# Kernel optimization log

Measured on AMD Instinct MI355X. Metric: run time of the kernel, lower is better.

## Reference

```python
import jax, jax.numpy as jnp
import numpy as np

D_MODEL = 1024
NUM_HEADS = 16
D_K = D_MODEL // NUM_HEADS


def setup_inputs() -> dict:
    key = jax.random.key(0)
    ks = jax.random.split(key, 11)
    B, S, D = 4, 2048, D_MODEL
    scale = 1.0 / np.sqrt(D)
    return {
        "Q": jax.random.normal(ks[0], (B, S, D), jnp.float32),
        "K": jax.random.normal(ks[1], (B, S, D), jnp.float32),
        "V": jax.random.normal(ks[2], (B, S, D), jnp.float32),
        "Wq": jax.random.normal(ks[3], (D, D), jnp.float32) * scale,
        "bq": jnp.zeros((D,), jnp.float32),
        "Wk": jax.random.normal(ks[4], (D, D), jnp.float32) * scale,
        "bk": jnp.zeros((D,), jnp.float32),
        "Wv": jax.random.normal(ks[5], (D, D), jnp.float32) * scale,
        "bv": jnp.zeros((D,), jnp.float32),
        "Wo": jax.random.normal(ks[6], (D, D), jnp.float32) * scale,
        "bo": jnp.zeros((D,), jnp.float32),
    }


def reference(Q, K, V, Wq, bq, Wk, bk, Wv, bv, Wo, bo):
    B, S, D = Q.shape
    H, Dk = NUM_HEADS, D_K
    # projections: [B,S,D] -> [B,H,S,Dk]
    def proj(x, W, b):
        y = jnp.einsum('bsd,de->bse', x, W.T) + b  # torch Linear: x @ W.T + b
        return y.reshape(B, -1, H, Dk).transpose(0, 2, 1, 3)
    q = proj(Q, Wq, bq)
    k = proj(K, Wk, bk)
    v = proj(V, Wv, bv)
    scores = jnp.einsum('bhqd,bhkd->bhqk', q, k) / np.sqrt(Dk)  # [B,H,S,S]
    attn = jax.nn.softmax(scores, axis=-1)
    out = jnp.einsum('bhqk,bhkd->bhqd', attn, v)  # [B,H,S,Dk]
    out = out.transpose(0, 2, 1, 3).reshape(B, -1, D)
    return jnp.einsum('bsd,de->bse', out, Wo.T) + bo
```

## Files before the change

kernel.cpp:

```cpp
#include <hip/hip_runtime.h>


typedef __bf16 bhalf_t;
typedef __attribute__((ext_vector_type(8)))  __bf16 bf16x8;
typedef __attribute__((ext_vector_type(4)))  __bf16 bf16x4;
typedef __attribute__((ext_vector_type(4)))  float  f32x4;
typedef __attribute__((ext_vector_type(16))) float  f32x16;

typedef __attribute__((address_space(1))) void gvoid_t;
typedef __attribute__((address_space(3))) void lvoid_t;
#define GLD16(g, l) __builtin_amdgcn_global_load_lds((const gvoid_t*)(g), (lvoid_t*)(l), 16, 0, 0)

__global__ __launch_bounds__(256) void cvt_all(
    const float* __restrict__ Q, const float* __restrict__ Kin, const float* __restrict__ V,
    const float* __restrict__ Wq, const float* __restrict__ Wk, const float* __restrict__ Wv,
    const float* __restrict__ Wo,
    bhalf_t* __restrict__ Qb, bhalf_t* __restrict__ Kb, bhalf_t* __restrict__ Vb,
    bhalf_t* __restrict__ Wqb, bhalf_t* __restrict__ Wkb, bhalf_t* __restrict__ Wvb,
    bhalf_t* __restrict__ Wob)
{
  size_t t = (size_t)blockIdx.x * 256 + threadIdx.x;
  const float* src; bhalf_t* dst;
  if (t < 2097152)      { src = Q;   dst = Qb; }
  else if (t < 4194304) { src = Kin; dst = Kb; t -= 2097152; }
  else if (t < 6291456) { src = V;   dst = Vb; t -= 4194304; }
  else {
    t -= 6291456;
    int w = (int)(t >> 18); t &= 262143;
    src = (w == 0) ? Wq  : (w == 1) ? Wk  : (w == 2) ? Wv  : Wo;
    dst = (w == 0) ? Wqb : (w == 1) ? Wkb : (w == 2) ? Wvb : Wob;
  }
  float4 f = ((const float4*)src)[t];
  bf16x4 o;
  o.x = (bhalf_t)f.x; o.y = (bhalf_t)f.y; o.z = (bhalf_t)f.z; o.w = (bhalf_t)f.w;
  ((bf16x4*)dst)[t] = o;
}

__device__ __forceinline__ void gemm_core_128(
    const bhalf_t* __restrict__ A, const bhalf_t* __restrict__ B,
    int bm, int bn, bhalf_t* As, bhalf_t* Bs, f32x4 acc[4][4])
{
  const int tid = threadIdx.x, lane = tid & 63, wave = tid >> 6;
  const int wm = wave >> 1, wn = wave & 1;
  const int quad = lane >> 4, tn = lane & 15;
  const int srow = lane >> 2, scol = (lane & 3) * 8;

  const bhalf_t* Ab0 = A + (size_t)(bm * 128 + wave * 16 + srow) * 1024 + scol;
  const bhalf_t* Ab1 = Ab0 + (size_t)64 * 1024;
  const bhalf_t* Bb0 = B + (size_t)(bn * 128 + wave * 16 + srow) * 1024 + scol;
  const bhalf_t* Bb1 = Bb0 + (size_t)64 * 1024;
  bhalf_t* Asw0 = As + wave * 512;  bhalf_t* Asw1 = As + (wave + 4) * 512;
  bhalf_t* Bsw0 = Bs + wave * 512;  bhalf_t* Bsw1 = Bs + (wave + 4) * 512;

  for (int k0 = 0; k0 < 1024; k0 += 32) {
    GLD16(Ab0 + k0, Asw0);
    GLD16(Ab1 + k0, Asw1);
    GLD16(Bb0 + k0, Bsw0);
    GLD16(Bb1 + k0, Bsw1);
    __syncthreads();
    bf16x8 af[4], bfr[4];
#pragma unroll
    for (int i = 0; i < 4; ++i)
      af[i] = *(const bf16x8*)(As + (wm * 64 + i * 16 + tn) * 32 + quad * 8);
#pragma unroll
    for (int j = 0; j < 4; ++j)
      bfr[j] = *(const bf16x8*)(Bs + (wn * 64 + j * 16 + tn) * 32 + quad * 8);
#pragma unroll
    for (int i = 0; i < 4; ++i)
#pragma unroll
      for (int j = 0; j < 4; ++j)
        acc[i][j] = __builtin_amdgcn_mfma_f32_16x16x32_bf16(af[i], bfr[j], acc[i][j], 0, 0, 0);
    __syncthreads();
  }
}

__global__ __launch_bounds__(256) void proj_gemm(
    const bhalf_t* __restrict__ Qb, const bhalf_t* __restrict__ Kb, const bhalf_t* __restrict__ Vb,
    const bhalf_t* __restrict__ Wqb, const bhalf_t* __restrict__ Wkb, const bhalf_t* __restrict__ Wvb,
    const float* __restrict__ bq, const float* __restrict__ bk, const float* __restrict__ bv,
    bhalf_t* __restrict__ qo, bhalf_t* __restrict__ ko, bhalf_t* __restrict__ vto)
{
  __shared__ bhalf_t As[4096];
  __shared__ bhalf_t Bs[4096];
  const int seg = blockIdx.x >> 9;
  const int idx = blockIdx.x & 511;
  const int bm = idx & 63, bn = idx >> 6;

  const bhalf_t *A, *Bw; const float* bias; bhalf_t* out; float scale; int mode;
  if (seg == 0)      { A = Qb; Bw = Wqb; bias = bq; out = qo;  scale = 0.18033688f; mode = 0; }
  else if (seg == 1) { A = Kb; Bw = Wkb; bias = bk; out = ko;  scale = 1.0f;        mode = 0; }
  else               { A = Vb; Bw = Wvb; bias = bv; out = vto; scale = 1.0f;        mode = 1; }

  f32x4 acc[4][4];
#pragma unroll
  for (int i = 0; i < 4; ++i)
#pragma unroll
    for (int j = 0; j < 4; ++j)
      acc[i][j] = (f32x4){0.f, 0.f, 0.f, 0.f};

  gemm_core_128(A, Bw, bm, bn, As, Bs, acc);

  const int lane = threadIdx.x & 63, wave = threadIdx.x >> 6;
  const int wm = wave >> 1, wn = wave & 1, quad = lane >> 4, tn = lane & 15;
#pragma unroll
  for (int i = 0; i < 4; ++i)
#pragma unroll
    for (int j = 0; j < 4; ++j) {
      const int n = bn * 128 + wn * 64 + j * 16 + tn;
      const float bsv = bias[n];
      const int h = n >> 6, dk = n & 63;
#pragma unroll
      for (int r = 0; r < 4; ++r) {
        const int m = bm * 128 + wm * 64 + i * 16 + quad * 4 + r;
        const int b = m >> 11, s = m & 2047;
        const float v = (acc[i][j][r] + bsv) * scale;
        size_t addr;
        if (mode == 0) addr = (((size_t)(b * 16 + h)) * 2048 + s) * 64 + dk;
        else {
          const int s2 = (s & ~12) | ((s & 4) << 1) | ((s & 8) >> 1);
          addr = (((size_t)(b * 16 + h)) * 64 + dk) * 2048 + s2;
        }
        out[addr] = (bhalf_t)v;
      }
    }
}

__global__ __launch_bounds__(256) void out_gemm(
    const bhalf_t* __restrict__ A, const bhalf_t* __restrict__ Bw,
    const float* __restrict__ bias, float* __restrict__ Cout)
{
  __shared__ bhalf_t As[4096];
  __shared__ bhalf_t Bs[4096];
  const int bm = blockIdx.x & 63, bn = blockIdx.x >> 6;

  f32x4 acc[4][4];
#pragma unroll
  for (int i = 0; i < 4; ++i)
#pragma unroll
    for (int j = 0; j < 4; ++j)
      acc[i][j] = (f32x4){0.f, 0.f, 0.f, 0.f};

  gemm_core_128(A, Bw, bm, bn, As, Bs, acc);

  const int lane = threadIdx.x & 63, wave = threadIdx.x >> 6;
  const int wm = wave >> 1, wn = wave & 1, quad = lane >> 4, tn = lane & 15;
#pragma unroll
  for (int i = 0; i < 4; ++i)
#pragma unroll
    for (int j = 0; j < 4; ++j) {
      const int n = bn * 128 + wn * 64 + j * 16 + tn;
      const float bsv = bias[n];
#pragma unroll
      for (int r = 0; r < 4; ++r) {
        const int m = bm * 128 + wm * 64 + i * 16 + quad * 4 + r;
        Cout[(size_t)m * 1024 + n] = acc[i][j][r] + bsv;
      }
    }
}

__global__ __launch_bounds__(256, 2) void attn_kernel(
    const bhalf_t* __restrict__ qp, const bhalf_t* __restrict__ kp,
    const bhalf_t* __restrict__ vtp, bhalf_t* __restrict__ outp)
{
  __shared__ bhalf_t Klds[4096];
  __shared__ bhalf_t Vtlds[4096];

  const int tid = threadIdx.x, lane = tid & 63, wave = tid >> 6;
  const int q31 = lane & 31, h = lane >> 5;
  const int bh = blockIdx.y, qt = blockIdx.x;

  const bhalf_t* qbase = qp + (((size_t)bh * 2048) + qt * 256 + wave * 64 + q31) * 64;
  bf16x8 qf[2][4];
#pragma unroll
  for (int qs = 0; qs < 2; ++qs)
#pragma unroll
    for (int ks = 0; ks < 4; ++ks)
      qf[qs][ks] = *(const bf16x8*)(qbase + qs * 32 * 64 + ks * 16 + h * 8);

  f32x16 Ot[2][2];
#pragma unroll
  for (int qs = 0; qs < 2; ++qs)
#pragma unroll
    for (int dd = 0; dd < 2; ++dd)
#pragma unroll
      for (int i = 0; i < 16; ++i) Ot[qs][dd][i] = 0.f;
  float Lp[2] = {0.f, 0.f};

  const bhalf_t* kbase  = kp  + (size_t)bh * 2048 * 64;
  const bhalf_t* vtbase = vtp + (size_t)bh * 64 * 2048;

  const int rloc = lane >> 3;
  const int cg8  = ((lane & 7) ^ rloc) * 8;
  const int q7 = q31 & 7;

  for (int kv0 = 0; kv0 < 2048; kv0 += 64) {
#pragma unroll
    for (int i = 0; i < 2; ++i) {
      const int r0 = (wave * 2 + i) * 8;
      GLD16(kbase + (size_t)(kv0 + r0 + rloc) * 64 + cg8, Klds + r0 * 64);
      GLD16(vtbase + (size_t)(r0 + rloc) * 2048 + kv0 + cg8, Vtlds + r0 * 64);
    }
    __syncthreads();

    bf16x8 pb[2][4];
#pragma unroll
    for (int mb = 0; mb < 2; ++mb) {
      bf16x8 ka[4];
#pragma unroll
      for (int ks = 0; ks < 4; ++ks)
        ka[ks] = *(const bf16x8*)(Klds + (mb * 32 + q31) * 64 + ((2 * ks + h) ^ q7) * 8);
#pragma unroll
      for (int qs = 0; qs < 2; ++qs) {
        f32x16 S;
#pragma unroll
        for (int i = 0; i < 16; ++i) S[i] = 0.f;
#pragma unroll
        for (int ks = 0; ks < 4; ++ks)
          S = __builtin_amdgcn_mfma_f32_32x32x16_bf16(ka[ks], qf[qs][ks], S, 0, 0, 0);
        float ls = 0.f;
#pragma unroll
        for (int half = 0; half < 2; ++half) {
          bf16x8 pk;
#pragma unroll
          for (int j = 0; j < 8; ++j) {
            const float e = __builtin_amdgcn_exp2f(S[half * 8 + j]);
            ls += e;
            pk[j] = (bhalf_t)e;
          }
          pb[qs][mb * 2 + half] = pk;
        }
        Lp[qs] += ls;
      }
    }

#pragma unroll
    for (int dd = 0; dd < 2; ++dd)
#pragma unroll
      for (int kb = 0; kb < 4; ++kb) {
        const bf16x8 va = *(const bf16x8*)(Vtlds + (dd * 32 + q31) * 64 + ((2 * kb + h) ^ q7) * 8);
#pragma unroll
        for (int qs = 0; qs < 2; ++qs)
          Ot[qs][dd] = __builtin_amdgcn_mfma_f32_32x32x16_bf16(va, pb[qs][kb], Ot[qs][dd], 0, 0, 0);
      }
    __syncthreads();
  }

  const int b = bh >> 4, hh = bh & 15;
#pragma unroll
  for (int qs = 0; qs < 2; ++qs) {
    const float Lt = Lp[qs] + __shfl_xor(Lp[qs], 32, 64);
    const float linv = 1.0f / Lt;
    const int s = qt * 256 + wave * 64 + qs * 32 + q31;
    bhalf_t* ob = outp + ((size_t)(b * 2048 + s)) * 1024 + hh * 64;
#pragma unroll
    for (int dd = 0; dd < 2; ++dd)
#pragma unroll
      for (int g = 0; g < 4; ++g) {
        bf16x4 o;
        o.x = (bhalf_t)(Ot[qs][dd][4 * g + 0] * linv);
        o.y = (bhalf_t)(Ot[qs][dd][4 * g + 1] * linv);
        o.z = (bhalf_t)(Ot[qs][dd][4 * g + 2] * linv);
        o.w = (bhalf_t)(Ot[qs][dd][4 * g + 3] * linv);
        *(bf16x4*)(ob + dd * 32 + g * 8 + h * 4) = o;
      }
  }
}

extern "C" void kernel_launch(void* const* d_in, const int* in_sizes, int n_in,
                              void* d_out, int out_size, void* d_ws, size_t ws_size,
                              hipStream_t stream)
{
  const float* Q  = (const float*)d_in[0];
  const float* K  = (const float*)d_in[1];
  const float* V  = (const float*)d_in[2];
  const float* Wq = (const float*)d_in[3];
  const float* bq = (const float*)d_in[4];
  const float* Wk = (const float*)d_in[5];
  const float* bk = (const float*)d_in[6];
  const float* Wv = (const float*)d_in[7];
  const float* bv = (const float*)d_in[8];
  const float* Wo = (const float*)d_in[9];
  const float* bo = (const float*)d_in[10];

  char* ws = (char*)d_ws;
  const size_t SZ = 8192ull * 1024 * 2;
  const size_t WZ = 1024ull * 1024 * 2;
  bhalf_t* Qb   = (bhalf_t*)(ws);
  bhalf_t* Kb   = (bhalf_t*)(ws + SZ);
  bhalf_t* Vb   = (bhalf_t*)(ws + 2 * SZ);
  bhalf_t* Wqb  = (bhalf_t*)(ws + 3 * SZ);
  bhalf_t* Wkb  = (bhalf_t*)(ws + 3 * SZ + WZ);
  bhalf_t* Wvb  = (bhalf_t*)(ws + 3 * SZ + 2 * WZ);
  bhalf_t* Wob  = (bhalf_t*)(ws + 3 * SZ + 3 * WZ);
  bhalf_t* q_p  = (bhalf_t*)(ws + 3 * SZ + 4 * WZ);
  bhalf_t* k_p  = (bhalf_t*)(ws + 4 * SZ + 4 * WZ);
  bhalf_t* vt_p = (bhalf_t*)(ws + 5 * SZ + 4 * WZ);
  bhalf_t* attn_o = Qb;

  cvt_all<<<28672, 256, 0, stream>>>(Q, K, V, Wq, Wk, Wv, Wo,
                                     Qb, Kb, Vb, Wqb, Wkb, Wvb, Wob);
  proj_gemm<<<1536, 256, 0, stream>>>(Qb, Kb, Vb, Wqb, Wkb, Wvb,
                                      bq, bk, bv, q_p, k_p, vt_p);
  attn_kernel<<<dim3(8, 64), 256, 0, stream>>>(q_p, k_p, vt_p, attn_o);
  out_gemm<<<512, 256, 0, stream>>>(attn_o, Wob, bo, (float*)d_out);
}
```

Before: 334.7 us.

## Fuse activation fp32->bf16 conversion into projection GEMM and double-buffer LDS

```diff
diff --git a/kernel.cpp b/kernel.cpp
--- a/kernel.cpp
+++ b/kernel.cpp
@@ -11,97 +11,102 @@
 typedef __attribute__((address_space(3))) void lvoid_t;
 #define GLD16(g, l) __builtin_amdgcn_global_load_lds((const gvoid_t*)(g), (lvoid_t*)(l), 16, 0, 0)
 
-__global__ __launch_bounds__(256) void cvt_all(
-    const float* __restrict__ Q, const float* __restrict__ Kin, const float* __restrict__ V,
-    const float* __restrict__ Wq, const float* __restrict__ Wk, const float* __restrict__ Wv,
-    const float* __restrict__ Wo,
-    bhalf_t* __restrict__ Qb, bhalf_t* __restrict__ Kb, bhalf_t* __restrict__ Vb,
-    bhalf_t* __restrict__ Wqb, bhalf_t* __restrict__ Wkb, bhalf_t* __restrict__ Wvb,
-    bhalf_t* __restrict__ Wob)
+__global__ __launch_bounds__(256) void cvt_w(
+    const float* __restrict__ Wq, const float* __restrict__ Wk,
+    const float* __restrict__ Wv, const float* __restrict__ Wo,
+    bhalf_t* __restrict__ Wqb, bhalf_t* __restrict__ Wkb,
+    bhalf_t* __restrict__ Wvb, bhalf_t* __restrict__ Wob)
 {
   size_t t = (size_t)blockIdx.x * 256 + threadIdx.x;
-  const float* src; bhalf_t* dst;
-  if (t < 2097152)      { src = Q;   dst = Qb; }
-  else if (t < 4194304) { src = Kin; dst = Kb; t -= 2097152; }
-  else if (t < 6291456) { src = V;   dst = Vb; t -= 4194304; }
-  else {
-    t -= 6291456;
-    int w = (int)(t >> 18); t &= 262143;
-    src = (w == 0) ? Wq  : (w == 1) ? Wk  : (w == 2) ? Wv  : Wo;
-    dst = (w == 0) ? Wqb : (w == 1) ? Wkb : (w == 2) ? Wvb : Wob;
-  }
+  int w = (int)(t >> 18); t &= 262143;
+  const float* src = (w == 0) ? Wq  : (w == 1) ? Wk  : (w == 2) ? Wv  : Wo;
+  bhalf_t*     dst = (w == 0) ? Wqb : (w == 1) ? Wkb : (w == 2) ? Wvb : Wob;
   float4 f = ((const float4*)src)[t];
   bf16x4 o;
   o.x = (bhalf_t)f.x; o.y = (bhalf_t)f.y; o.z = (bhalf_t)f.z; o.w = (bhalf_t)f.w;
   ((bf16x4*)dst)[t] = o;
 }
 
-__device__ __forceinline__ void gemm_core_128(
-    const bhalf_t* __restrict__ A, const bhalf_t* __restrict__ B,
-    int bm, int bn, bhalf_t* As, bhalf_t* Bs, f32x4 acc[4][4])
-{
+__global__ __launch_bounds__(256) void proj_gemm(
+    const float* __restrict__ Qf, const float* __restrict__ Kf, const float* __restrict__ Vf,
+    const bhalf_t* __restrict__ Wqb, const bhalf_t* __restrict__ Wkb, const bhalf_t* __restrict__ Wvb,
+    const float* __restrict__ bq, const float* __restrict__ bk, const float* __restrict__ bv,
+    bhalf_t* __restrict__ qo, bhalf_t* __restrict__ ko, bhalf_t* __restrict__ vto)
+{
+  __shared__ float   AsF[2][4096];
+  __shared__ bhalf_t Bs [2][4096];
+
+  const int seg = blockIdx.x >> 9;
+  const int idx = blockIdx.x & 511;
+  const int bm = idx & 63, bn = idx >> 6;
+
+  const float *A; const bhalf_t *Bw; const float* bias; bhalf_t* out; float scale; int mode;
+  if (seg == 0)      { A = Qf; Bw = Wqb; bias = bq; out = qo;  scale = 0.18033688f; mode = 0; }
+  else if (seg == 1) { A = Kf; Bw = Wkb; bias = bk; out = ko;  scale = 1.0f;        mode = 0; }
+  else               { A = Vf; Bw = Wvb; bias = bv; out = vto; scale = 1.0f;        mode = 1; }
+
   const int tid = threadIdx.x, lane = tid & 63, wave = tid >> 6;
   const int wm = wave >> 1, wn = wave & 1;
   const int quad = lane >> 4, tn = lane & 15;
-  const int srow = lane >> 2, scol = (lane & 3) * 8;
-
-  const bhalf_t* Ab0 = A + (size_t)(bm * 128 + wave * 16 + srow) * 1024 + scol;
-  const bhalf_t* Ab1 = Ab0 + (size_t)64 * 1024;
-  const bhalf_t* Bb0 = B + (size_t)(bn * 128 + wave * 16 + srow) * 1024 + scol;
-  const bhalf_t* Bb1 = Bb0 + (size_t)64 * 1024;
-  bhalf_t* Asw0 = As + wave * 512;  bhalf_t* Asw1 = As + (wave + 4) * 512;
-  bhalf_t* Bsw0 = Bs + wave * 512;  bhalf_t* Bsw1 = Bs + (wave + 4) * 512;
-
+
+  const int ar = lane >> 3;
+  const int ac = ((lane & 7) ^ ar) * 4;
+  const int br = lane >> 2;
+  const int bc = ((lane & 3) ^ (br & 3)) * 8;
+
+  const float*   Ag = A  + (size_t)(bm * 128 + ar) * 1024 + ac;
+  const bhalf_t* Bg = Bw + (size_t)(bn * 128 + br) * 1024 + bc;
+
+  auto stage = [&](int k0, int buf) {
+#pragma unroll
+    for (int i = 0; i < 4; ++i)
+      GLD16(Ag + (size_t)(wave * 32 + i * 8) * 1024 + k0, &AsF[buf][(wave * 32 + i * 8) * 32]);
+#pragma unroll
+    for (int i = 0; i < 2; ++i) {
+      const int c = wave * 2 + i;
+      GLD16(Bg + (size_t)(c * 16) * 1024 + k0, &Bs[buf][c * 16 * 32]);
+    }
+  };
+
+  f32x4 acc[4][4];
+#pragma unroll
+  for (int i = 0; i < 4; ++i)
+#pragma unroll
+    for (int j = 0; j < 4; ++j)
+      acc[i][j] = (f32x4){0.f, 0.f, 0.f, 0.f};
+
+  stage(0, 0);
   for (int k0 = 0; k0 < 1024; k0 += 32) {
-    GLD16(Ab0 + k0, Asw0);
-    GLD16(Ab1 + k0, Asw1);
-    GLD16(Bb0 + k0, Bsw0);
-    GLD16(Bb1 + k0, Bsw1);
+    const int buf = (k0 >> 5) & 1;
     __syncthreads();
+    if (k0 + 32 < 1024) stage(k0 + 32, buf ^ 1);
+
+    const float*   Ab = AsF[buf];
+    const bhalf_t* Bb = Bs[buf];
     bf16x8 af[4], bfr[4];
 #pragma unroll
-    for (int i = 0; i < 4; ++i)
-      af[i] = *(const bf16x8*)(As + (wm * 64 + i * 16 + tn) * 32 + quad * 8);
-#pragma unroll
-    for (int j = 0; j < 4; ++j)
-      bfr[j] = *(const bf16x8*)(Bs + (wn * 64 + j * 16 + tn) * 32 + quad * 8);
+    for (int i = 0; i < 4; ++i) {
+      const int r = wm * 64 + i * 16 + tn;
+      const int r7 = tn & 7;
+      const f32x4 u0 = *(const f32x4*)(Ab + r * 32 + ((2 * quad) ^ r7) * 4);
+      const f32x4 u1 = *(const f32x4*)(Ab + r * 32 + ((2 * quad + 1) ^ r7) * 4);
+      bf16x8 t;
+      t[0] = (bhalf_t)u0.x; t[1] = (bhalf_t)u0.y; t[2] = (bhalf_t)u0.z; t[3] = (bhalf_t)u0.w;
+      t[4] = (bhalf_t)u1.x; t[5] = (bhalf_t)u1.y; t[6] = (bhalf_t)u1.z; t[7] = (bhalf_t)u1.w;
+      af[i] = t;
+    }
+#pragma unroll
+    for (int j = 0; j < 4; ++j) {
+      const int r = wn * 64 + j * 16 + tn;
+      bfr[j] = *(const bf16x8*)(Bb + r * 32 + (quad ^ (tn & 3)) * 8);
+    }
 #pragma unroll
     for (int i = 0; i < 4; ++i)
 #pragma unroll
       for (int j = 0; j < 4; ++j)
         acc[i][j] = __builtin_amdgcn_mfma_f32_16x16x32_bf16(af[i], bfr[j], acc[i][j], 0, 0, 0);
-    __syncthreads();
   }
-}
-
-__global__ __launch_bounds__(256) void proj_gemm(
-    const bhalf_t* __restrict__ Qb, const bhalf_t* __restrict__ Kb, const bhalf_t* __restrict__ Vb,
-    const bhalf_t* __restrict__ Wqb, const bhalf_t* __restrict__ Wkb, const bhalf_t* __restrict__ Wvb,
-    const float* __restrict__ bq, const float* __restrict__ bk, const float* __restrict__ bv,
-    bhalf_t* __restrict__ qo, bhalf_t* __restrict__ ko, bhalf_t* __restrict__ vto)
-{
-  __shared__ bhalf_t As[4096];
-  __shared__ bhalf_t Bs[4096];
-  const int seg = blockIdx.x >> 9;
-  const int idx = blockIdx.x & 511;
-  const int bm = idx & 63, bn = idx >> 6;
-
-  const bhalf_t *A, *Bw; const float* bias; bhalf_t* out; float scale; int mode;
-  if (seg == 0)      { A = Qb; Bw = Wqb; bias = bq; out = qo;  scale = 0.18033688f; mode = 0; }
-  else if (seg == 1) { A = Kb; Bw = Wkb; bias = bk; out = ko;  scale = 1.0f;        mode = 0; }
-  else               { A = Vb; Bw = Wvb; bias = bv; out = vto; scale = 1.0f;        mode = 1; }
-
-  f32x4 acc[4][4];
-#pragma unroll
-  for (int i = 0; i < 4; ++i)
-#pragma unroll
-    for (int j = 0; j < 4; ++j)
-      acc[i][j] = (f32x4){0.f, 0.f, 0.f, 0.f};
-
-  gemm_core_128(A, Bw, bm, bn, As, Bs, acc);
-
-  const int lane = threadIdx.x & 63, wave = threadIdx.x >> 6;
-  const int wm = wave >> 1, wn = wave & 1, quad = lane >> 4, tn = lane & 15;
+
 #pragma unroll
   for (int i = 0; i < 4; ++i)
 #pragma unroll
@@ -129,9 +134,27 @@
     const bhalf_t* __restrict__ A, const bhalf_t* __restrict__ Bw,
     const float* __restrict__ bias, float* __restrict__ Cout)
 {
-  __shared__ bhalf_t As[4096];
-  __shared__ bhalf_t Bs[4096];
+  __shared__ bhalf_t As[2][4096];
+  __shared__ bhalf_t Bs[2][4096];
   const int bm = blockIdx.x & 63, bn = blockIdx.x >> 6;
+
+  const int tid = threadIdx.x, lane = tid & 63, wave = tid >> 6;
+  const int wm = wave >> 1, wn = wave & 1;
+  const int quad = lane >> 4, tn = lane & 15;
+
+  const int br = lane >> 2;
+  const int bc = ((lane & 3) ^ (br & 3)) * 8;
+  const bhalf_t* Ag = A  + (size_t)(bm * 128 + br) * 1024 + bc;
+  const bhalf_t* Bg = Bw + (size_t)(bn * 128 + br) * 1024 + bc;
+
+  auto stage = [&](int k0, int buf) {
+#pragma unroll
+    for (int i = 0; i < 2; ++i) {
+      const int c = wave * 2 + i;
+      GLD16(Ag + (size_t)(c * 16) * 1024 + k0, &As[buf][c * 16 * 32]);
+      GLD16(Bg + (size_t)(c * 16) * 1024 + k0, &Bs[buf][c * 16 * 32]);
+    }
+  };
 
   f32x4 acc[4][4];
 #pragma unroll
@@ -140,10 +163,32 @@
     for (int j = 0; j < 4; ++j)
       acc[i][j] = (f32x4){0.f, 0.f, 0.f, 0.f};
 
-  gemm_core_128(A, Bw, bm, bn, As, Bs, acc);
-
-  const int lane = threadIdx.x & 63, wave = threadIdx.x >> 6;
-  const int wm = wave >> 1, wn = wave & 1, quad = lane >> 4, tn = lane & 15;
+  stage(0, 0);
+  for (int k0 = 0; k0 < 1024; k0 += 32) {
+    const int buf = (k0 >> 5) & 1;
+    __syncthreads();
+    if (k0 + 32 < 1024) stage(k0 + 32, buf ^ 1);
+
+    const bhalf_t* Ab = As[buf];
+    const bhalf_t* Bb = Bs[buf];
+    bf16x8 af[4], bfr[4];
+#pragma unroll
+    for (int i = 0; i < 4; ++i) {
+      const int r = wm * 64 + i * 16 + tn;
+      af[i] = *(const bf16x8*)(Ab + r * 32 + (quad ^ (tn & 3)) * 8);
+    }
+#pragma unroll
+    for (int j = 0; j < 4; ++j) {
+      const int r = wn * 64 + j * 16 + tn;
+      bfr[j] = *(const bf16x8*)(Bb + r * 32 + (quad ^ (tn & 3)) * 8);
+    }
+#pragma unroll
+    for (int i = 0; i < 4; ++i)
+#pragma unroll
+      for (int j = 0; j < 4; ++j)
+        acc[i][j] = __builtin_amdgcn_mfma_f32_16x16x32_bf16(af[i], bfr[j], acc[i][j], 0, 0, 0);
+  }
+
 #pragma unroll
   for (int i = 0; i < 4; ++i)
 #pragma unroll
@@ -162,8 +207,8 @@
     const bhalf_t* __restrict__ qp, const bhalf_t* __restrict__ kp,
     const bhalf_t* __restrict__ vtp, bhalf_t* __restrict__ outp)
 {
-  __shared__ bhalf_t Klds[4096];
-  __shared__ bhalf_t Vtlds[4096];
+  __shared__ bhalf_t Klds [2][4096];
+  __shared__ bhalf_t Vtlds[2][4096];
 
   const int tid = threadIdx.x, lane = tid & 63, wave = tid >> 6;
   const int q31 = lane & 31, h = lane >> 5;
@@ -193,14 +238,23 @@
   const int cg8  = ((lane & 7) ^ rloc) * 8;
   const int q7 = q31 & 7;
 
-  for (int kv0 = 0; kv0 < 2048; kv0 += 64) {
+  auto stage = [&](int kv0, int buf) {
 #pragma unroll
     for (int i = 0; i < 2; ++i) {
       const int r0 = (wave * 2 + i) * 8;
-      GLD16(kbase + (size_t)(kv0 + r0 + rloc) * 64 + cg8, Klds + r0 * 64);
-      GLD16(vtbase + (size_t)(r0 + rloc) * 2048 + kv0 + cg8, Vtlds + r0 * 64);
-    }
+      GLD16(kbase + (size_t)(kv0 + r0 + rloc) * 64 + cg8, &Klds[buf][r0 * 64]);
+      GLD16(vtbase + (size_t)(r0 + rloc) * 2048 + kv0 + cg8, &Vtlds[buf][r0 * 64]);
+    }
+  };
+
+  stage(0, 0);
+  for (int kv0 = 0; kv0 < 2048; kv0 += 64) {
+    const int buf = (kv0 >> 6) & 1;
     __syncthreads();
+    if (kv0 + 64 < 2048) stage(kv0 + 64, buf ^ 1);
+
+    const bhalf_t* Kb  = Klds[buf];
+    const bhalf_t* Vtb = Vtlds[buf];
 
     bf16x8 pb[2][4];
 #pragma unroll
@@ -208,7 +262,7 @@
       bf16x8 ka[4];
 #pragma unroll
       for (int ks = 0; ks < 4; ++ks)
-        ka[ks] = *(const bf16x8*)(Klds + (mb * 32 + q31) * 64 + ((2 * ks + h) ^ q7) * 8);
+        ka[ks] = *(const bf16x8*)(Kb + (mb * 32 + q31) * 64 + ((2 * ks + h) ^ q7) * 8);
 #pragma unroll
       for (int qs = 0; qs < 2; ++qs) {
         f32x16 S;
@@ -237,12 +291,11 @@
     for (int dd = 0; dd < 2; ++dd)
 #pragma unroll
       for (int kb = 0; kb < 4; ++kb) {
-        const bf16x8 va = *(const bf16x8*)(Vtlds + (dd * 32 + q31) * 64 + ((2 * kb + h) ^ q7) * 8);
+        const bf16x8 va = *(const bf16x8*)(Vtb + (dd * 32 + q31) * 64 + ((2 * kb + h) ^ q7) * 8);
 #pragma unroll
         for (int qs = 0; qs < 2; ++qs)
           Ot[qs][dd] = __builtin_amdgcn_mfma_f32_32x32x16_bf16(va, pb[qs][kb], Ot[qs][dd], 0, 0, 0);
       }
-    __syncthreads();
   }
 
   const int b = bh >> 4, hh = bh & 15;
@@ -285,21 +338,17 @@
   char* ws = (char*)d_ws;
   const size_t SZ = 8192ull * 1024 * 2;
   const size_t WZ = 1024ull * 1024 * 2;
-  bhalf_t* Qb   = (bhalf_t*)(ws);
-  bhalf_t* Kb   = (bhalf_t*)(ws + SZ);
-  bhalf_t* Vb   = (bhalf_t*)(ws + 2 * SZ);
-  bhalf_t* Wqb  = (bhalf_t*)(ws + 3 * SZ);
-  bhalf_t* Wkb  = (bhalf_t*)(ws + 3 * SZ + WZ);
-  bhalf_t* Wvb  = (bhalf_t*)(ws + 3 * SZ + 2 * WZ);
-  bhalf_t* Wob  = (bhalf_t*)(ws + 3 * SZ + 3 * WZ);
-  bhalf_t* q_p  = (bhalf_t*)(ws + 3 * SZ + 4 * WZ);
-  bhalf_t* k_p  = (bhalf_t*)(ws + 4 * SZ + 4 * WZ);
-  bhalf_t* vt_p = (bhalf_t*)(ws + 5 * SZ + 4 * WZ);
-  bhalf_t* attn_o = Qb;
-
-  cvt_all<<<28672, 256, 0, stream>>>(Q, K, V, Wq, Wk, Wv, Wo,
-                                     Qb, Kb, Vb, Wqb, Wkb, Wvb, Wob);
-  proj_gemm<<<1536, 256, 0, stream>>>(Qb, Kb, Vb, Wqb, Wkb, Wvb,
+  bhalf_t* Wqb    = (bhalf_t*)(ws);
+  bhalf_t* Wkb    = (bhalf_t*)(ws + WZ);
+  bhalf_t* Wvb    = (bhalf_t*)(ws + 2 * WZ);
+  bhalf_t* Wob    = (bhalf_t*)(ws + 3 * WZ);
+  bhalf_t* q_p    = (bhalf_t*)(ws + 4 * WZ);
+  bhalf_t* k_p    = (bhalf_t*)(ws + 4 * WZ + SZ);
+  bhalf_t* vt_p   = (bhalf_t*)(ws + 4 * WZ + 2 * SZ);
+  bhalf_t* attn_o = (bhalf_t*)(ws + 4 * WZ + 3 * SZ);
+
+  cvt_w<<<4096, 256, 0, stream>>>(Wq, Wk, Wv, Wo, Wqb, Wkb, Wvb, Wob);
+  proj_gemm<<<1536, 256, 0, stream>>>(Q, K, V, Wqb, Wkb, Wvb,
                                       bq, bk, bv, q_p, k_p, vt_p);
   attn_kernel<<<dim3(8, 64), 256, 0, stream>>>(q_p, k_p, vt_p, attn_o);
   out_gemm<<<512, 256, 0, stream>>>(attn_o, Wob, bo, (float*)d_out);
```

New measurement: 348.7 us. 1.04x slower.

## Double-buffer LDS tiles in GEMMs and attention; swizzle GEMM LDS layout

Applied to the files above, without the earlier changes.

```diff
diff --git a/kernel.cpp b/kernel.cpp
--- a/kernel.cpp
+++ b/kernel.cpp
@@ -36,52 +36,15 @@
   ((bf16x4*)dst)[t] = o;
 }
 
-__device__ __forceinline__ void gemm_core_128(
-    const bhalf_t* __restrict__ A, const bhalf_t* __restrict__ B,
-    int bm, int bn, bhalf_t* As, bhalf_t* Bs, f32x4 acc[4][4])
-{
-  const int tid = threadIdx.x, lane = tid & 63, wave = tid >> 6;
-  const int wm = wave >> 1, wn = wave & 1;
-  const int quad = lane >> 4, tn = lane & 15;
-  const int srow = lane >> 2, scol = (lane & 3) * 8;
-
-  const bhalf_t* Ab0 = A + (size_t)(bm * 128 + wave * 16 + srow) * 1024 + scol;
-  const bhalf_t* Ab1 = Ab0 + (size_t)64 * 1024;
-  const bhalf_t* Bb0 = B + (size_t)(bn * 128 + wave * 16 + srow) * 1024 + scol;
-  const bhalf_t* Bb1 = Bb0 + (size_t)64 * 1024;
-  bhalf_t* Asw0 = As + wave * 512;  bhalf_t* Asw1 = As + (wave + 4) * 512;
-  bhalf_t* Bsw0 = Bs + wave * 512;  bhalf_t* Bsw1 = Bs + (wave + 4) * 512;
-
-  for (int k0 = 0; k0 < 1024; k0 += 32) {
-    GLD16(Ab0 + k0, Asw0);
-    GLD16(Ab1 + k0, Asw1);
-    GLD16(Bb0 + k0, Bsw0);
-    GLD16(Bb1 + k0, Bsw1);
-    __syncthreads();
-    bf16x8 af[4], bfr[4];
-#pragma unroll
-    for (int i = 0; i < 4; ++i)
-      af[i] = *(const bf16x8*)(As + (wm * 64 + i * 16 + tn) * 32 + quad * 8);
-#pragma unroll
-    for (int j = 0; j < 4; ++j)
-      bfr[j] = *(const bf16x8*)(Bs + (wn * 64 + j * 16 + tn) * 32 + quad * 8);
-#pragma unroll
-    for (int i = 0; i < 4; ++i)
-#pragma unroll
-      for (int j = 0; j < 4; ++j)
-        acc[i][j] = __builtin_amdgcn_mfma_f32_16x16x32_bf16(af[i], bfr[j], acc[i][j], 0, 0, 0);
-    __syncthreads();
-  }
-}
-
-__global__ __launch_bounds__(256) void proj_gemm(
+__global__ __launch_bounds__(256, 5) void proj_gemm(
     const bhalf_t* __restrict__ Qb, const bhalf_t* __restrict__ Kb, const bhalf_t* __restrict__ Vb,
     const bhalf_t* __restrict__ Wqb, const bhalf_t* __restrict__ Wkb, const bhalf_t* __restrict__ Wvb,
     const float* __restrict__ bq, const float* __restrict__ bk, const float* __restrict__ bv,
     bhalf_t* __restrict__ qo, bhalf_t* __restrict__ ko, bhalf_t* __restrict__ vto)
 {
-  __shared__ bhalf_t As[4096];
-  __shared__ bhalf_t Bs[4096];
+  __shared__ bhalf_t As[2][4096];
+  __shared__ bhalf_t Bs[2][4096];
+
   const int seg = blockIdx.x >> 9;
   const int idx = blockIdx.x & 511;
   const int bm = idx & 63, bn = idx >> 6;
@@ -91,6 +54,24 @@
   else if (seg == 1) { A = Kb; Bw = Wkb; bias = bk; out = ko;  scale = 1.0f;        mode = 0; }
   else               { A = Vb; Bw = Wvb; bias = bv; out = vto; scale = 1.0f;        mode = 1; }
 
+  const int tid = threadIdx.x, lane = tid & 63, wave = tid >> 6;
+  const int wm = wave >> 1, wn = wave & 1;
+  const int quad = lane >> 4, tn = lane & 15;
+  const int srow = lane >> 2;
+  const int scol = ((lane & 3) ^ (srow & 3)) * 8;
+
+  const bhalf_t* Ab0 = A + (size_t)(bm * 128 + wave * 16 + srow) * 1024 + scol;
+  const bhalf_t* Ab1 = Ab0 + (size_t)64 * 1024;
+  const bhalf_t* Bb0 = Bw + (size_t)(bn * 128 + wave * 16 + srow) * 1024 + scol;
+  const bhalf_t* Bb1 = Bb0 + (size_t)64 * 1024;
+
+  auto stage = [&](int k0, int buf) {
+    GLD16(Ab0 + k0, &As[buf][wave * 512]);
+    GLD16(Ab1 + k0, &As[buf][(wave + 4) * 512]);
+    GLD16(Bb0 + k0, &Bs[buf][wave * 512]);
+    GLD16(Bb1 + k0, &Bs[buf][(wave + 4) * 512]);
+  };
+
   f32x4 acc[4][4];
 #pragma unroll
   for (int i = 0; i < 4; ++i)
@@ -98,10 +79,30 @@
     for (int j = 0; j < 4; ++j)
       acc[i][j] = (f32x4){0.f, 0.f, 0.f, 0.f};
 
-  gemm_core_128(A, Bw, bm, bn, As, Bs, acc);
-
-  const int lane = threadIdx.x & 63, wave = threadIdx.x >> 6;
-  const int wm = wave >> 1, wn = wave & 1, quad = lane >> 4, tn = lane & 15;
+  stage(0, 0);
+  for (int k0 = 0; k0 < 1024; k0 += 32) {
+    const int buf = (k0 >> 5) & 1;
+    __syncthreads();
+    if (k0 + 32 < 1024) stage(k0 + 32, buf ^ 1);
+
+    bf16x8 af[4], bfr[4];
+#pragma unroll
+    for (int i = 0; i < 4; ++i) {
+      const int r = wm * 64 + i * 16 + tn;
+      af[i] = *(const bf16x8*)(&As[buf][r * 32 + (quad ^ (tn & 3)) * 8]);
+    }
+#pragma unroll
+    for (int j = 0; j < 4; ++j) {
+      const int r = wn * 64 + j * 16 + tn;
+      bfr[j] = *(const bf16x8*)(&Bs[buf][r * 32 + (quad ^ (tn & 3)) * 8]);
+    }
+#pragma unroll
+    for (int i = 0; i < 4; ++i)
+#pragma unroll
+      for (int j = 0; j < 4; ++j)
+        acc[i][j] = __builtin_amdgcn_mfma_f32_16x16x32_bf16(af[i], bfr[j], acc[i][j], 0, 0, 0);
+  }
+
 #pragma unroll
   for (int i = 0; i < 4; ++i)
 #pragma unroll
@@ -125,13 +126,31 @@
     }
 }
 
-__global__ __launch_bounds__(256) void out_gemm(
+__global__ __launch_bounds__(256, 5) void out_gemm(
     const bhalf_t* __restrict__ A, const bhalf_t* __restrict__ Bw,
     const float* __restrict__ bias, float* __restrict__ Cout)
 {
-  __shared__ bhalf_t As[4096];
-  __shared__ bhalf_t Bs[4096];
+  __shared__ bhalf_t As[2][4096];
+  __shared__ bhalf_t Bs[2][4096];
   const int bm = blockIdx.x & 63, bn = blockIdx.x >> 6;
+
+  const int tid = threadIdx.x, lane = tid & 63, wave = tid >> 6;
+  const int wm = wave >> 1, wn = wave & 1;
+  const int quad = lane >> 4, tn = lane & 15;
+  const int srow = lane >> 2;
+  const int scol = ((lane & 3) ^ (srow & 3)) * 8;
+
+  const bhalf_t* Ab0 = A  + (size_t)(bm * 128 + wave * 16 + srow) * 1024 + scol;
+  const bhalf_t* Ab1 = Ab0 + (size_t)64 * 1024;
+  const bhalf_t* Bb0 = Bw + (size_t)(bn * 128 + wave * 16 + srow) * 1024 + scol;
+  const bhalf_t* Bb1 = Bb0 + (size_t)64 * 1024;
+
+  auto stage = [&](int k0, int buf) {
+    GLD16(Ab0 + k0, &As[buf][wave * 512]);
+    GLD16(Ab1 + k0, &As[buf][(wave + 4) * 512]);
+    GLD16(Bb0 + k0, &Bs[buf][wave * 512]);
+    GLD16(Bb1 + k0, &Bs[buf][(wave + 4) * 512]);
+  };
 
   f32x4 acc[4][4];
 #pragma unroll
@@ -140,10 +159,30 @@
     for (int j = 0; j < 4; ++j)
       acc[i][j] = (f32x4){0.f, 0.f, 0.f, 0.f};
 
-  gemm_core_128(A, Bw, bm, bn, As, Bs, acc);
-
-  const int lane = threadIdx.x & 63, wave = threadIdx.x >> 6;
-  const int wm = wave >> 1, wn = wave & 1, quad = lane >> 4, tn = lane & 15;
+  stage(0, 0);
+  for (int k0 = 0; k0 < 1024; k0 += 32) {
+    const int buf = (k0 >> 5) & 1;
+    __syncthreads();
+    if (k0 + 32 < 1024) stage(k0 + 32, buf ^ 1);
+
+    bf16x8 af[4], bfr[4];
+#pragma unroll
+    for (int i = 0; i < 4; ++i) {
+      const int r = wm * 64 + i * 16 + tn;
+      af[i] = *(const bf16x8*)(&As[buf][r * 32 + (quad ^ (tn & 3)) * 8]);
+    }
+#pragma unroll
+    for (int j = 0; j < 4; ++j) {
+      const int r = wn * 64 + j * 16 + tn;
+      bfr[j] = *(const bf16x8*)(&Bs[buf][r * 32 + (quad ^ (tn & 3)) * 8]);
+    }
+#pragma unroll
+    for (int i = 0; i < 4; ++i)
+#pragma unroll
+      for (int j = 0; j < 4; ++j)
+        acc[i][j] = __builtin_amdgcn_mfma_f32_16x16x32_bf16(af[i], bfr[j], acc[i][j], 0, 0, 0);
+  }
+
 #pragma unroll
   for (int i = 0; i < 4; ++i)
 #pragma unroll
@@ -162,8 +201,8 @@
     const bhalf_t* __restrict__ qp, const bhalf_t* __restrict__ kp,
     const bhalf_t* __restrict__ vtp, bhalf_t* __restrict__ outp)
 {
-  __shared__ bhalf_t Klds[4096];
-  __shared__ bhalf_t Vtlds[4096];
+  __shared__ bhalf_t Klds [2][4096];
+  __shared__ bhalf_t Vtlds[2][4096];
 
   const int tid = threadIdx.x, lane = tid & 63, wave = tid >> 6;
   const int q31 = lane & 31, h = lane >> 5;
@@ -193,14 +232,23 @@
   const int cg8  = ((lane & 7) ^ rloc) * 8;
   const int q7 = q31 & 7;
 
-  for (int kv0 = 0; kv0 < 2048; kv0 += 64) {
+  auto stage = [&](int kv0, int buf) {
 #pragma unroll
     for (int i = 0; i < 2; ++i) {
       const int r0 = (wave * 2 + i) * 8;
-      GLD16(kbase + (size_t)(kv0 + r0 + rloc) * 64 + cg8, Klds + r0 * 64);
-      GLD16(vtbase + (size_t)(r0 + rloc) * 2048 + kv0 + cg8, Vtlds + r0 * 64);
-    }
+      GLD16(kbase + (size_t)(kv0 + r0 + rloc) * 64 + cg8, &Klds[buf][r0 * 64]);
+      GLD16(vtbase + (size_t)(r0 + rloc) * 2048 + kv0 + cg8, &Vtlds[buf][r0 * 64]);
+    }
+  };
+
+  stage(0, 0);
+  for (int kv0 = 0; kv0 < 2048; kv0 += 64) {
+    const int buf = (kv0 >> 6) & 1;
     __syncthreads();
+    if (kv0 + 64 < 2048) stage(kv0 + 64, buf ^ 1);
+
+    const bhalf_t* Kb  = Klds[buf];
+    const bhalf_t* Vtb = Vtlds[buf];
 
     bf16x8 pb[2][4];
 #pragma unroll
@@ -208,7 +256,7 @@
       bf16x8 ka[4];
 #pragma unroll
       for (int ks = 0; ks < 4; ++ks)
-        ka[ks] = *(const bf16x8*)(Klds + (mb * 32 + q31) * 64 + ((2 * ks + h) ^ q7) * 8);
+        ka[ks] = *(const bf16x8*)(Kb + (mb * 32 + q31) * 64 + ((2 * ks + h) ^ q7) * 8);
 #pragma unroll
       for (int qs = 0; qs < 2; ++qs) {
         f32x16 S;
@@ -237,12 +285,11 @@
     for (int dd = 0; dd < 2; ++dd)
 #pragma unroll
       for (int kb = 0; kb < 4; ++kb) {
-        const bf16x8 va = *(const bf16x8*)(Vtlds + (dd * 32 + q31) * 64 + ((2 * kb + h) ^ q7) * 8);
+        const bf16x8 va = *(const bf16x8*)(Vtb + (dd * 32 + q31) * 64 + ((2 * kb + h) ^ q7) * 8);
 #pragma unroll
         for (int qs = 0; qs < 2; ++qs)
           Ot[qs][dd] = __builtin_amdgcn_mfma_f32_32x32x16_bf16(va, pb[qs][kb], Ot[qs][dd], 0, 0, 0);
       }
-    __syncthreads();
   }
 
   const int b = bh >> 4, hh = bh & 15;
```

Result: slower. 551.0 us (+64.6%).
